# Kernel optimization log

Hardware: AMD Instinct MI355X
Metric: run time of the kernel (lower is better)

The kernel has to match this reference:

```python
import jax, jax.numpy as jnp
import numpy as np

F = 256   # nb_features
H = 8     # nb_heads
B = 4
S = 1024  # q_s == kv_s
SCALE = F ** 0.5  # module MULTIPLIES scores by sqrt(f) when scale=True


def setup_inputs() -> dict:
    key = jax.random.key(0)
    ks = jax.random.split(key, 6)
    return {
        "q_input": jax.random.normal(ks[0], (B, F, S), dtype=jnp.float32),
        "kv_input": jax.random.normal(ks[1], (B, F, S), dtype=jnp.float32),
        "Wq": jax.random.normal(ks[2], (F, F * H), dtype=jnp.float32) * (F ** -0.5),
        "Wk": jax.random.normal(ks[3], (F, F * H), dtype=jnp.float32) * (F ** -0.5),
        "Wv": jax.random.normal(ks[4], (F, F * H), dtype=jnp.float32) * (F ** -0.5),
        "Wz": jax.random.normal(ks[5], (F * H, F), dtype=jnp.float32) * ((F * H) ** -0.5),
    }


def reference(q_input, kv_input, Wq, Wk, Wv, Wz):
    b, f, q_s = q_input.shape
    kv_s = kv_input.shape[2]
    h = H
    # (b, f, s) -> (b, s, f)
    qx = jnp.transpose(q_input, (0, 2, 1))
    kvx = jnp.transpose(kv_input, (0, 2, 1))
    # Linear f -> f*h, then split last dim into (f, h)
    q = (qx @ Wq).reshape(b, q_s, f, h)
    k = (kvx @ Wk).reshape(b, kv_s, f, h)
    v = (kvx @ Wv).reshape(b, kv_s, f, h)
    # sigmoid-gated attention: scores MULTIPLIED by sqrt(f)
    qkt = jnp.einsum('bifh,bjfh->bijh', q, k)
    attn = jax.nn.sigmoid(qkt * SCALE)
    weighted_v = jnp.einsum('bijh,bjfh->bifh', attn, v)  # (b, q_s, f, h)
    z = weighted_v.reshape(b * q_s, f * h)
    out = jax.nn.relu(z @ Wz)  # dropout p=0.0 -> identity
    return jnp.transpose(out.reshape(b, q_s, f), (0, 2, 1))  # (b, f, q_s)
```

## Files before the change

### kernel.cpp

```cpp
#include <hip/hip_runtime.h>
#include <hip/hip_fp16.h>

typedef _Float16 f16;
typedef _Float16 f16x8 __attribute__((ext_vector_type(8)));
typedef float f32x4 __attribute__((ext_vector_type(4)));

#define AS1(p) ((const __attribute__((address_space(1))) void*)(p))
#define AS3(p) ((__attribute__((address_space(3))) void*)(p))

__device__ __forceinline__ void gload16(const void* g, void* l) {
  __builtin_amdgcn_global_load_lds(AS1(g), AS3(l), 16, 0, 0);
}

__global__ __launch_bounds__(256) void tkern(const float* __restrict__ in,
                                             f16* __restrict__ out,
                                             long in_rs, long in_bs,
                                             long out_rs, long out_bs) {
  __shared__ float t[64][68];
  const float* ip = in + blockIdx.z * in_bs + (long)(blockIdx.y * 64) * in_rs + blockIdx.x * 64;
  f16* op = out + blockIdx.z * out_bs + (long)(blockIdx.x * 64) * out_rs + blockIdx.y * 64;
  int tid = threadIdx.x;
  {
    int c4 = (tid & 15) * 4, r0 = tid >> 4;
#pragma unroll
    for (int p = 0; p < 4; ++p) {
      int r = r0 + 16 * p;
      float4 v = *(const float4*)(ip + (long)r * in_rs + c4);
      t[c4 + 0][r] = v.x; t[c4 + 1][r] = v.y; t[c4 + 2][r] = v.z; t[c4 + 3][r] = v.w;
    }
  }
  __syncthreads();
  {
    int r4 = (tid & 15) * 4, c0 = tid >> 4;
#pragma unroll
    for (int p = 0; p < 4; ++p) {
      int c = c0 + 16 * p;
      float4 v = *(const float4*)(&t[c][r4]);
      union { f16 h[4]; unsigned long long u; } pk;
      pk.h[0] = (f16)v.x; pk.h[1] = (f16)v.y; pk.h[2] = (f16)v.z; pk.h[3] = (f16)v.w;
      *(unsigned long long*)(op + (long)c * out_rs + r4) = pk.u;
    }
  }
}

__global__ __launch_bounds__(256) void projk(
    const f16* __restrict__ Xq, const f16* __restrict__ Xkv,
    const f16* __restrict__ Wqt, const f16* __restrict__ Wkt, const f16* __restrict__ Wvt,
    f16* __restrict__ Qh, f16* __restrict__ Kh, f16* __restrict__ Vt) {
  __shared__ char sm[34816];
  int z = blockIdx.z;
  const f16* A = (z == 0) ? Xq : Xkv;
  const f16* B = (z == 0) ? Wqt : (z == 1) ? Wkt : Wvt;
  int m0 = blockIdx.x * 128, n0 = blockIdx.y * 128;
  int tid = threadIdx.x, wave = tid >> 6, lane = tid & 63;
  int wm = wave & 1, wn = wave >> 1;
  char* As = sm;
  char* Bs = sm + 16384;
  f32x4 acc[4][4];
#pragma unroll
  for (int i = 0; i < 4; ++i)
#pragma unroll
    for (int j = 0; j < 4; ++j) acc[i][j] = (f32x4){0.f, 0.f, 0.f, 0.f};

  for (int kt = 0; kt < 4; ++kt) {
    int k0 = kt * 64;
    __syncthreads();
#pragma unroll
    for (int is = 0; is < 4; ++is) {
      int loff = is * 4096 + wave * 1024;
      int g = loff + lane * 16;
      int row = g >> 7, sl = (g >> 4) & 7;
      int sp = (sl ^ (row & 7)) * 8;
      gload16(A + (long)(m0 + row) * 256 + k0 + sp, As + loff);
      gload16(B + (long)(n0 + row) * 256 + k0 + sp, Bs + loff);
    }
    __syncthreads();
#pragma unroll
    for (int t = 0; t < 2; ++t) {
      f16x8 af[4], bf[4];
#pragma unroll
      for (int mi = 0; mi < 4; ++mi) {
        int row = wm * 64 + mi * 16 + (lane & 15);
        int sl = (t * 4 + (lane >> 4)) ^ (row & 7);
        af[mi] = *(const f16x8*)(As + row * 128 + sl * 16);
      }
#pragma unroll
      for (int ni = 0; ni < 4; ++ni) {
        int row = wn * 64 + ni * 16 + (lane & 15);
        int sl = (t * 4 + (lane >> 4)) ^ (row & 7);
        bf[ni] = *(const f16x8*)(Bs + row * 128 + sl * 16);
      }
#pragma unroll
      for (int mi = 0; mi < 4; ++mi)
#pragma unroll
        for (int ni = 0; ni < 4; ++ni)
          acc[mi][ni] = __builtin_amdgcn_mfma_f32_16x16x32_f16(af[mi], bf[ni], acc[mi][ni], 0, 0, 0);
    }
  }
  __syncthreads();
#pragma unroll
  for (int mi = 0; mi < 4; ++mi)
#pragma unroll
    for (int ni = 0; ni < 4; ++ni) {
      int cc = wn * 64 + ni * 16 + (lane & 15);
      int rs0 = wm * 64 + mi * 16 + (lane >> 4) * 4;
      union { f16 h[4]; unsigned long long u; } pk;
#pragma unroll
      for (int r = 0; r < 4; ++r) pk.h[r] = (f16)acc[mi][ni][r];
      *(unsigned long long*)(sm + cc * 272 + rs0 * 2) = pk.u;
    }
  __syncthreads();
  if (z < 2) {
    f16* outp = (z == 0) ? Qh : Kh;
#pragma unroll
    for (int pass = 0; pass < 4; ++pass) {
      int item = pass * 256 + tid;
      int rs = item & 127, h = item >> 7;
      int m = m0 + rs, b = m >> 10, s = m & 1023;
      union { unsigned short u16[16]; uint4 q[2]; } pk;
#pragma unroll
      for (int u = 0; u < 16; ++u)
        pk.u16[u] = *(const unsigned short*)(sm + (h + 8 * u) * 272 + rs * 2);
      f16* dst = outp + ((long)(b * 8 + h) * 1024 + s) * 256 + (n0 >> 3);
      *(uint4*)dst = pk.q[0];
      *(uint4*)(dst + 8) = pk.q[1];
    }
  } else {
    int cc = tid >> 1, half = tid & 1;
    int c = n0 + cc, h = c & 7, fi = c >> 3;
    int m = m0 + half * 64;
    int b = m >> 10, s0 = m & 1023;
    uint4 q[8];
#pragma unroll
    for (int j = 0; j < 8; ++j)
      q[j] = *(const uint4*)(sm + cc * 272 + half * 128 + j * 16);
    f16* dst = Vt + ((long)(b * 8 + h) * 256 + fi) * 1024 + s0;
#pragma unroll
    for (int j = 0; j < 8; ++j) *(uint4*)(dst + j * 8) = q[j];
  }
}

__global__ __launch_bounds__(256) void attnk(
    const f16* __restrict__ Qh, const f16* __restrict__ Kh,
    const f16* __restrict__ Vt, f16* __restrict__ Zb) {
  __shared__ char sm[36864];
  char* Ks = sm;
  char* Vs = sm + 16384;
  char* Ps = sm + 32768;
  int flat = blockIdx.x;
  int xcd = flat & 7, slotb = flat >> 3;
  int bh = xcd + 8 * (slotb & 3);
  int i0 = (slotb >> 2) * 64;
  int tid = threadIdx.x, wave = tid >> 6, lane = tid & 63;
  const f16* Qp = Qh + (long)bh * 262144;
  const f16* Kp = Kh + (long)bh * 262144;
  const f16* Vp = Vt + (long)bh * 262144;
  f16x8 q[8];
  {
    const f16* qr = Qp + (long)(i0 + wave * 16 + (lane & 15)) * 256 + (lane >> 4) * 8;
#pragma unroll
    for (int t = 0; t < 8; ++t) q[t] = *(const f16x8*)(qr + t * 32);
  }
  f32x4 acc[4][4];
#pragma unroll
  for (int i = 0; i < 4; ++i)
#pragma unroll
    for (int j = 0; j < 4; ++j) acc[i][j] = (f32x4){0.f, 0.f, 0.f, 0.f};

  for (int jt = 0; jt < 32; ++jt) {
    int j0 = jt * 32;
    __syncthreads();
#pragma unroll
    for (int is = 0; is < 4; ++is) {
      int loff = is * 4096 + wave * 1024;
      int g = loff + lane * 16;
      {
        int row = g >> 9, sl = (g >> 4) & 31;
        gload16(Kp + (long)(j0 + row) * 256 + ((sl ^ (row & 7)) * 8), Ks + loff);
      }
      {
        int row = g >> 6, sl = (g >> 4) & 3;
        gload16(Vp + (long)row * 1024 + j0 + ((sl ^ ((row >> 1) & 3)) * 8), Vs + loff);
      }
    }
    __syncthreads();
    f32x4 accs[2];
    accs[0] = (f32x4){0.f, 0.f, 0.f, 0.f};
    accs[1] = (f32x4){0.f, 0.f, 0.f, 0.f};
#pragma unroll
    for (int t = 0; t < 8; ++t) {
#pragma unroll
      for (int jf = 0; jf < 2; ++jf) {
        int jr = jf * 16 + (lane & 15);
        int sl = (t * 4 + (lane >> 4)) ^ (jr & 7);
        f16x8 kf = *(const f16x8*)(Ks + jr * 512 + sl * 16);
        accs[jf] = __builtin_amdgcn_mfma_f32_16x16x32_f16(q[t], kf, accs[jf], 0, 0, 0);
      }
    }
#pragma unroll
    for (int jf = 0; jf < 2; ++jf) {
      int j = jf * 16 + (lane & 15);
#pragma unroll
      for (int r = 0; r < 4; ++r) {
        int i = wave * 16 + (lane >> 4) * 4 + r;
        float x = accs[jf][r];
        float p = __builtin_amdgcn_rcpf(1.0f + __builtin_amdgcn_exp2f(x * -23.083120654223414f));
        *(f16*)(Ps + i * 64 + ((j * 2) ^ (((i >> 1) & 3) << 4))) = (f16)p;
      }
    }
    __syncthreads();
    f16x8 pa[4];
#pragma unroll
    for (int mi = 0; mi < 4; ++mi) {
      int ir = mi * 16 + (lane & 15);
      int sl = (lane >> 4) ^ ((ir >> 1) & 3);
      pa[mi] = *(const f16x8*)(Ps + ir * 64 + sl * 16);
    }
#pragma unroll
    for (int nf = 0; nf < 4; ++nf) {
      int fr = wave * 64 + nf * 16 + (lane & 15);
      int sl = (lane >> 4) ^ ((fr >> 1) & 3);
      f16x8 vb = *(const f16x8*)(Vs + fr * 64 + sl * 16);
#pragma unroll
      for (int mi = 0; mi < 4; ++mi)
        acc[mi][nf] = __builtin_amdgcn_mfma_f32_16x16x32_f16(pa[mi], vb, acc[mi][nf], 0, 0, 0);
    }
  }
  f16* zp = Zb + ((long)bh * 1024 + i0) * 256;
#pragma unroll
  for (int mi = 0; mi < 4; ++mi)
#pragma unroll
    for (int nf = 0; nf < 4; ++nf)
#pragma unroll
      for (int r = 0; r < 4; ++r) {
        int i = mi * 16 + (lane >> 4) * 4 + r;
        int f = wave * 64 + nf * 16 + (lane & 15);
        zp[(long)i * 256 + f] = (f16)acc[mi][nf][r];
      }
}

__global__ __launch_bounds__(256) void zkern(
    const f16* __restrict__ Wzt, const f16* __restrict__ Zb,
    float* __restrict__ out) {
  __shared__ char sm[16384];
  char* As = sm;
  char* Bs = sm + 8192;
  int fo0 = blockIdx.x * 64, s0 = blockIdx.y * 64, b = blockIdx.z;
  int tid = threadIdx.x, wave = tid >> 6, lane = tid & 63;
  int wm = wave & 1, wn = wave >> 1;
  f32x4 acc[2][2];
#pragma unroll
  for (int i = 0; i < 2; ++i)
#pragma unroll
    for (int j = 0; j < 2; ++j) acc[i][j] = (f32x4){0.f, 0.f, 0.f, 0.f};

  for (int kt = 0; kt < 32; ++kt) {
    int k0 = kt * 64, h = k0 >> 8, fi0 = k0 & 255;
    __syncthreads();
#pragma unroll
    for (int is = 0; is < 2; ++is) {
      int loff = is * 4096 + wave * 1024;
      int g = loff + lane * 16;
      int row = g >> 7, sl = (g >> 4) & 7;
      int sp = (sl ^ (row & 7)) * 8;
      gload16(Wzt + (long)(fo0 + row) * 2048 + k0 + sp, As + loff);
      gload16(Zb + ((long)(b * 8 + h) * 1024 + s0 + row) * 256 + fi0 + sp, Bs + loff);
    }
    __syncthreads();
#pragma unroll
    for (int t = 0; t < 2; ++t) {
      f16x8 af[2], bf[2];
#pragma unroll
      for (int mi = 0; mi < 2; ++mi) {
        int row = wm * 32 + mi * 16 + (lane & 15);
        int sl = (t * 4 + (lane >> 4)) ^ (row & 7);
        af[mi] = *(const f16x8*)(As + row * 128 + sl * 16);
      }
#pragma unroll
      for (int ni = 0; ni < 2; ++ni) {
        int row = wn * 32 + ni * 16 + (lane & 15);
        int sl = (t * 4 + (lane >> 4)) ^ (row & 7);
        bf[ni] = *(const f16x8*)(Bs + row * 128 + sl * 16);
      }
#pragma unroll
      for (int mi = 0; mi < 2; ++mi)
#pragma unroll
        for (int ni = 0; ni < 2; ++ni)
          acc[mi][ni] = __builtin_amdgcn_mfma_f32_16x16x32_f16(af[mi], bf[ni], acc[mi][ni], 0, 0, 0);
    }
  }
#pragma unroll
  for (int mi = 0; mi < 2; ++mi)
#pragma unroll
    for (int ni = 0; ni < 2; ++ni)
#pragma unroll
      for (int r = 0; r < 4; ++r) {
        int fo = fo0 + wm * 32 + mi * 16 + (lane >> 4) * 4 + r;
        int s = s0 + wn * 32 + ni * 16 + (lane & 15);
        float v = acc[mi][ni][r];
        out[((long)b * 256 + fo) * 1024 + s] = v > 0.f ? v : 0.f;
      }
}

extern "C" void kernel_launch(void* const* d_in, const int* in_sizes, int n_in,
                              void* d_out, int out_size, void* d_ws, size_t ws_size,
                              hipStream_t stream) {
  const float* qin = (const float*)d_in[0];
  const float* kvin = (const float*)d_in[1];
  const float* Wq = (const float*)d_in[2];
  const float* Wk = (const float*)d_in[3];
  const float* Wv = (const float*)d_in[4];
  const float* Wz = (const float*)d_in[5];
  float* out = (float*)d_out;
  char* ws = (char*)d_ws;
  const long MB = 1 << 20;
  f16* Xq  = (f16*)(ws + 0 * MB);
  f16* Xkv = (f16*)(ws + 2 * MB);
  f16* Wqt = (f16*)(ws + 4 * MB);
  f16* Wkt = (f16*)(ws + 5 * MB);
  f16* Wvt = (f16*)(ws + 6 * MB);
  f16* Wzt = (f16*)(ws + 7 * MB);
  f16* Qh  = (f16*)(ws + 8 * MB);
  f16* Kh  = (f16*)(ws + 24 * MB);
  f16* Vt  = (f16*)(ws + 40 * MB);
  f16* Zb  = Qh;
  dim3 blk(256);
  tkern<<<dim3(16, 4, 4), blk, 0, stream>>>(qin, Xq, 1024L, 262144L, 256L, 262144L);
  tkern<<<dim3(16, 4, 4), blk, 0, stream>>>(kvin, Xkv, 1024L, 262144L, 256L, 262144L);
  tkern<<<dim3(32, 4, 1), blk, 0, stream>>>(Wq, Wqt, 2048L, 0L, 256L, 0L);
  tkern<<<dim3(32, 4, 1), blk, 0, stream>>>(Wk, Wkt, 2048L, 0L, 256L, 0L);
  tkern<<<dim3(32, 4, 1), blk, 0, stream>>>(Wv, Wvt, 2048L, 0L, 256L, 0L);
  tkern<<<dim3(4, 4, 8),  blk, 0, stream>>>(Wz, Wzt, 2048L, 256L, 2048L, 256L);
  projk<<<dim3(32, 16, 3), blk, 0, stream>>>(Xq, Xkv, Wqt, Wkt, Wvt, Qh, Kh, Vt);
  attnk<<<dim3(512), blk, 0, stream>>>(Qh, Kh, Vt, Zb);
  zkern<<<dim3(4, 16, 4), blk, 0, stream>>>(Wzt, Zb, out);
}
```

Measured before the change: 138.0 us.

## Double-buffer GEMM/attention tiles, keep P in registers, merge transpose launches

Adds LDS double buffering to the projection, attention and output GEMM kernels, so the next tile's global-to-LDS load overlaps the current tile's MFMAs and each iteration needs one barrier instead of two. The attention kernel is restructured: each wave now owns 16 query rows across all 256 features. The sigmoid probabilities are rearranged into the MFMA A-operand layout with permlane swaps instead of a round trip through LDS, and Z is written out through an LDS-staged coalesced store. The six transpose launches are merged into three. The costs are a larger LDS footprint per block (64KB), which may reduce occupancy, and more accumulator registers in attention.

```diff
diff --git a/kernel.cpp b/kernel.cpp
--- a/kernel.cpp
+++ b/kernel.cpp
@@ -12,13 +12,20 @@
   __builtin_amdgcn_global_load_lds(AS1(g), AS3(l), 16, 0, 0);
 }
 
-__global__ __launch_bounds__(256) void tkern(const float* __restrict__ in,
-                                             f16* __restrict__ out,
-                                             long in_rs, long in_bs,
-                                             long out_rs, long out_bs) {
+__device__ __forceinline__ float sgm(float x) {
+  return __builtin_amdgcn_rcpf(1.0f + __builtin_amdgcn_exp2f(x * -23.083120654223414f));
+}
+
+__device__ __forceinline__ unsigned pack2(float a, float b) {
+  union { f16 h[2]; unsigned u; } x;
+  x.h[0] = (f16)a; x.h[1] = (f16)b;
+  return x.u;
+}
+
+__device__ __forceinline__ void tbody(const float* __restrict__ ip,
+                                      f16* __restrict__ op,
+                                      long in_rs, long out_rs) {
   __shared__ float t[64][68];
-  const float* ip = in + blockIdx.z * in_bs + (long)(blockIdx.y * 64) * in_rs + blockIdx.x * 64;
-  f16* op = out + blockIdx.z * out_bs + (long)(blockIdx.x * 64) * out_rs + blockIdx.y * 64;
   int tid = threadIdx.x;
   {
     int c4 = (tid & 15) * 4, r0 = tid >> 4;
@@ -43,28 +50,60 @@
   }
 }
 
+__global__ __launch_bounds__(256) void tin(const float* __restrict__ qin,
+                                           const float* __restrict__ kvin,
+                                           f16* __restrict__ Xq, f16* __restrict__ Xkv) {
+  int z = blockIdx.z;
+  const float* in = (z < 4) ? qin : kvin;
+  f16* out = (z < 4) ? Xq : Xkv;
+  long b = z & 3;
+  tbody(in + b * 262144 + (long)(blockIdx.y * 64) * 1024 + blockIdx.x * 64,
+        out + b * 262144 + (long)(blockIdx.x * 64) * 256 + blockIdx.y * 64,
+        1024, 256);
+}
+
+__global__ __launch_bounds__(256) void tw3(const float* __restrict__ Wq,
+                                           const float* __restrict__ Wk,
+                                           const float* __restrict__ Wv,
+                                           f16* __restrict__ Wqt, f16* __restrict__ Wkt,
+                                           f16* __restrict__ Wvt) {
+  int z = blockIdx.z;
+  const float* in = (z == 0) ? Wq : (z == 1) ? Wk : Wv;
+  f16* out = (z == 0) ? Wqt : (z == 1) ? Wkt : Wvt;
+  tbody(in + (long)(blockIdx.y * 64) * 2048 + blockIdx.x * 64,
+        out + (long)(blockIdx.x * 64) * 256 + blockIdx.y * 64,
+        2048, 256);
+}
+
+__global__ __launch_bounds__(256) void twz(const float* __restrict__ Wz,
+                                           f16* __restrict__ Wzt) {
+  long z = blockIdx.z;
+  tbody(Wz + z * 256 + (long)(blockIdx.y * 64) * 2048 + blockIdx.x * 64,
+        Wzt + z * 256 + (long)(blockIdx.x * 64) * 2048 + blockIdx.y * 64,
+        2048, 2048);
+}
+
 __global__ __launch_bounds__(256) void projk(
     const f16* __restrict__ Xq, const f16* __restrict__ Xkv,
     const f16* __restrict__ Wqt, const f16* __restrict__ Wkt, const f16* __restrict__ Wvt,
     f16* __restrict__ Qh, f16* __restrict__ Kh, f16* __restrict__ Vt) {
-  __shared__ char sm[34816];
+  __shared__ char sm[65536];
   int z = blockIdx.z;
   const f16* A = (z == 0) ? Xq : Xkv;
   const f16* B = (z == 0) ? Wqt : (z == 1) ? Wkt : Wvt;
   int m0 = blockIdx.x * 128, n0 = blockIdx.y * 128;
   int tid = threadIdx.x, wave = tid >> 6, lane = tid & 63;
   int wm = wave & 1, wn = wave >> 1;
-  char* As = sm;
-  char* Bs = sm + 16384;
   f32x4 acc[4][4];
 #pragma unroll
   for (int i = 0; i < 4; ++i)
 #pragma unroll
     for (int j = 0; j < 4; ++j) acc[i][j] = (f32x4){0.f, 0.f, 0.f, 0.f};
 
-  for (int kt = 0; kt < 4; ++kt) {
+  auto PSTAGE = [&](int buf, int kt) {
+    char* As = sm + buf * 32768;
+    char* Bs = As + 16384;
     int k0 = kt * 64;
-    __syncthreads();
 #pragma unroll
     for (int is = 0; is < 4; ++is) {
       int loff = is * 4096 + wave * 1024;
@@ -74,7 +113,15 @@
       gload16(A + (long)(m0 + row) * 256 + k0 + sp, As + loff);
       gload16(B + (long)(n0 + row) * 256 + k0 + sp, Bs + loff);
     }
-    __syncthreads();
+  };
+
+  PSTAGE(0, 0);
+  __syncthreads();
+  for (int kt = 0; kt < 4; ++kt) {
+    int cur = kt & 1;
+    if (kt < 3) PSTAGE(cur ^ 1, kt + 1);
+    const char* As = sm + cur * 32768;
+    const char* Bs = As + 16384;
 #pragma unroll
     for (int t = 0; t < 2; ++t) {
       f16x8 af[4], bf[4];
@@ -96,8 +143,8 @@
         for (int ni = 0; ni < 4; ++ni)
           acc[mi][ni] = __builtin_amdgcn_mfma_f32_16x16x32_f16(af[mi], bf[ni], acc[mi][ni], 0, 0, 0);
     }
-  }
-  __syncthreads();
+    __syncthreads();
+  }
 #pragma unroll
   for (int mi = 0; mi < 4; ++mi)
 #pragma unroll
@@ -143,33 +190,29 @@
 __global__ __launch_bounds__(256) void attnk(
     const f16* __restrict__ Qh, const f16* __restrict__ Kh,
     const f16* __restrict__ Vt, f16* __restrict__ Zb) {
-  __shared__ char sm[36864];
-  char* Ks = sm;
-  char* Vs = sm + 16384;
-  char* Ps = sm + 32768;
+  __shared__ char sm[65536];
   int flat = blockIdx.x;
   int xcd = flat & 7, slotb = flat >> 3;
   int bh = xcd + 8 * (slotb & 3);
   int i0 = (slotb >> 2) * 64;
   int tid = threadIdx.x, wave = tid >> 6, lane = tid & 63;
+  int l15 = lane & 15, l4 = lane >> 4;
   const f16* Qp = Qh + (long)bh * 262144;
   const f16* Kp = Kh + (long)bh * 262144;
   const f16* Vp = Vt + (long)bh * 262144;
   f16x8 q[8];
   {
-    const f16* qr = Qp + (long)(i0 + wave * 16 + (lane & 15)) * 256 + (lane >> 4) * 8;
+    const f16* qr = Qp + (long)(i0 + wave * 16 + l15) * 256 + l4 * 8;
 #pragma unroll
     for (int t = 0; t < 8; ++t) q[t] = *(const f16x8*)(qr + t * 32);
   }
-  f32x4 acc[4][4];
-#pragma unroll
-  for (int i = 0; i < 4; ++i)
-#pragma unroll
-    for (int j = 0; j < 4; ++j) acc[i][j] = (f32x4){0.f, 0.f, 0.f, 0.f};
-
-  for (int jt = 0; jt < 32; ++jt) {
-    int j0 = jt * 32;
-    __syncthreads();
+  f32x4 acc[16];
+#pragma unroll
+  for (int i = 0; i < 16; ++i) acc[i] = (f32x4){0.f, 0.f, 0.f, 0.f};
+
+  auto STAGE = [&](int buf, int j0) {
+    char* Ks = sm + buf * 32768;
+    char* Vs = Ks + 16384;
 #pragma unroll
     for (int is = 0; is < 4; ++is) {
       int loff = is * 4096 + wave * 1024;
@@ -183,68 +226,67 @@
         gload16(Vp + (long)row * 1024 + j0 + ((sl ^ ((row >> 1) & 3)) * 8), Vs + loff);
       }
     }
+  };
+
+  STAGE(0, 0);
+  __syncthreads();
+  for (int jt = 0; jt < 32; ++jt) {
+    int cur = jt & 1;
+    if (jt < 31) STAGE(cur ^ 1, (jt + 1) * 32);
+    const char* Ks = sm + cur * 32768;
+    const char* Vs = Ks + 16384;
+    f32x4 s0 = (f32x4){0.f, 0.f, 0.f, 0.f};
+    f32x4 s1 = (f32x4){0.f, 0.f, 0.f, 0.f};
+#pragma unroll
+    for (int t = 0; t < 8; ++t) {
+      int sl = (t * 4 + l4) ^ (l15 & 7);
+      f16x8 k0 = *(const f16x8*)(Ks + l15 * 512 + sl * 16);
+      f16x8 k1 = *(const f16x8*)(Ks + (16 + l15) * 512 + sl * 16);
+      s0 = __builtin_amdgcn_mfma_f32_16x16x32_f16(k0, q[t], s0, 0, 0, 0);
+      s1 = __builtin_amdgcn_mfma_f32_16x16x32_f16(k1, q[t], s1, 0, 0, 0);
+    }
+    unsigned u00 = pack2(sgm(s0[0]), sgm(s0[1]));
+    unsigned u01 = pack2(sgm(s0[2]), sgm(s0[3]));
+    unsigned u10 = pack2(sgm(s1[0]), sgm(s1[1]));
+    unsigned u11 = pack2(sgm(s1[2]), sgm(s1[3]));
+    auto a0 = __builtin_amdgcn_permlane32_swap(u00, u10, false, false);
+    auto w02 = __builtin_amdgcn_permlane16_swap(a0[0], a0[1], false, false);
+    auto a1 = __builtin_amdgcn_permlane32_swap(u01, u11, false, false);
+    auto w13 = __builtin_amdgcn_permlane16_swap(a1[0], a1[1], false, false);
+    union { unsigned u[4]; f16x8 v; } pa;
+    pa.u[0] = w02[0]; pa.u[1] = w13[0]; pa.u[2] = w02[1]; pa.u[3] = w13[1];
+#pragma unroll
+    for (int nf = 0; nf < 16; ++nf) {
+      int fr = nf * 16 + l15;
+      int sl = l4 ^ ((fr >> 1) & 3);
+      f16x8 vb = *(const f16x8*)(Vs + fr * 64 + sl * 16);
+      acc[nf] = __builtin_amdgcn_mfma_f32_16x16x32_f16(pa.v, vb, acc[nf], 0, 0, 0);
+    }
     __syncthreads();
-    f32x4 accs[2];
-    accs[0] = (f32x4){0.f, 0.f, 0.f, 0.f};
-    accs[1] = (f32x4){0.f, 0.f, 0.f, 0.f};
-#pragma unroll
-    for (int t = 0; t < 8; ++t) {
-#pragma unroll
-      for (int jf = 0; jf < 2; ++jf) {
-        int jr = jf * 16 + (lane & 15);
-        int sl = (t * 4 + (lane >> 4)) ^ (jr & 7);
-        f16x8 kf = *(const f16x8*)(Ks + jr * 512 + sl * 16);
-        accs[jf] = __builtin_amdgcn_mfma_f32_16x16x32_f16(q[t], kf, accs[jf], 0, 0, 0);
-      }
-    }
-#pragma unroll
-    for (int jf = 0; jf < 2; ++jf) {
-      int j = jf * 16 + (lane & 15);
-#pragma unroll
-      for (int r = 0; r < 4; ++r) {
-        int i = wave * 16 + (lane >> 4) * 4 + r;
-        float x = accs[jf][r];
-        float p = __builtin_amdgcn_rcpf(1.0f + __builtin_amdgcn_exp2f(x * -23.083120654223414f));
-        *(f16*)(Ps + i * 64 + ((j * 2) ^ (((i >> 1) & 3) << 4))) = (f16)p;
-      }
-    }
-    __syncthreads();
-    f16x8 pa[4];
-#pragma unroll
-    for (int mi = 0; mi < 4; ++mi) {
-      int ir = mi * 16 + (lane & 15);
-      int sl = (lane >> 4) ^ ((ir >> 1) & 3);
-      pa[mi] = *(const f16x8*)(Ps + ir * 64 + sl * 16);
-    }
-#pragma unroll
-    for (int nf = 0; nf < 4; ++nf) {
-      int fr = wave * 64 + nf * 16 + (lane & 15);
-      int sl = (lane >> 4) ^ ((fr >> 1) & 3);
-      f16x8 vb = *(const f16x8*)(Vs + fr * 64 + sl * 16);
-#pragma unroll
-      for (int mi = 0; mi < 4; ++mi)
-        acc[mi][nf] = __builtin_amdgcn_mfma_f32_16x16x32_f16(pa[mi], vb, acc[mi][nf], 0, 0, 0);
-    }
-  }
+  }
+#pragma unroll
+  for (int nf = 0; nf < 16; ++nf)
+#pragma unroll
+    for (int r = 0; r < 4; ++r) {
+      int il = wave * 16 + l4 * 4 + r;
+      int f = nf * 16 + l15;
+      *(f16*)(sm + il * 512 + ((f * 2) ^ (((il >> 2) & 3) << 5))) = (f16)acc[nf][r];
+    }
+  __syncthreads();
   f16* zp = Zb + ((long)bh * 1024 + i0) * 256;
 #pragma unroll
-  for (int mi = 0; mi < 4; ++mi)
-#pragma unroll
-    for (int nf = 0; nf < 4; ++nf)
-#pragma unroll
-      for (int r = 0; r < 4; ++r) {
-        int i = mi * 16 + (lane >> 4) * 4 + r;
-        int f = wave * 64 + nf * 16 + (lane & 15);
-        zp[(long)i * 256 + f] = (f16)acc[mi][nf][r];
-      }
+  for (int c = 0; c < 8; ++c) {
+    int il = c * 8 + (tid >> 5);
+    int fb = (tid & 31) * 16;
+    uint4 v = *(const uint4*)(sm + il * 512 + (fb ^ (((il >> 2) & 3) << 5)));
+    *(uint4*)((char*)zp + il * 512 + fb) = v;
+  }
 }
 
 __global__ __launch_bounds__(256) void zkern(
     const f16* __restrict__ Wzt, const f16* __restrict__ Zb,
     float* __restrict__ out) {
-  __shared__ char sm[16384];
-  char* As = sm;
-  char* Bs = sm + 8192;
+  __shared__ char sm[32768];
   int fo0 = blockIdx.x * 64, s0 = blockIdx.y * 64, b = blockIdx.z;
   int tid = threadIdx.x, wave = tid >> 6, lane = tid & 63;
   int wm = wave & 1, wn = wave >> 1;
@@ -254,9 +296,10 @@
 #pragma unroll
     for (int j = 0; j < 2; ++j) acc[i][j] = (f32x4){0.f, 0.f, 0.f, 0.f};
 
-  for (int kt = 0; kt < 32; ++kt) {
+  auto ZSTAGE = [&](int buf, int kt) {
+    char* As = sm + buf * 16384;
+    char* Bs = As + 8192;
     int k0 = kt * 64, h = k0 >> 8, fi0 = k0 & 255;
-    __syncthreads();
 #pragma unroll
     for (int is = 0; is < 2; ++is) {
       int loff = is * 4096 + wave * 1024;
@@ -266,7 +309,15 @@
       gload16(Wzt + (long)(fo0 + row) * 2048 + k0 + sp, As + loff);
       gload16(Zb + ((long)(b * 8 + h) * 1024 + s0 + row) * 256 + fi0 + sp, Bs + loff);
     }
-    __syncthreads();
+  };
+
+  ZSTAGE(0, 0);
+  __syncthreads();
+  for (int kt = 0; kt < 32; ++kt) {
+    int cur = kt & 1;
+    if (kt < 31) ZSTAGE(cur ^ 1, kt + 1);
+    const char* As = sm + cur * 16384;
+    const char* Bs = As + 8192;
 #pragma unroll
     for (int t = 0; t < 2; ++t) {
       f16x8 af[2], bf[2];
@@ -288,6 +339,7 @@
         for (int ni = 0; ni < 2; ++ni)
           acc[mi][ni] = __builtin_amdgcn_mfma_f32_16x16x32_f16(af[mi], bf[ni], acc[mi][ni], 0, 0, 0);
     }
+    __syncthreads();
   }
 #pragma unroll
   for (int mi = 0; mi < 2; ++mi)
@@ -325,12 +377,9 @@
   f16* Vt  = (f16*)(ws + 40 * MB);
   f16* Zb  = Qh;
   dim3 blk(256);
-  tkern<<<dim3(16, 4, 4), blk, 0, stream>>>(qin, Xq, 1024L, 262144L, 256L, 262144L);
-  tkern<<<dim3(16, 4, 4), blk, 0, stream>>>(kvin, Xkv, 1024L, 262144L, 256L, 262144L);
-  tkern<<<dim3(32, 4, 1), blk, 0, stream>>>(Wq, Wqt, 2048L, 0L, 256L, 0L);
-  tkern<<<dim3(32, 4, 1), blk, 0, stream>>>(Wk, Wkt, 2048L, 0L, 256L, 0L);
-  tkern<<<dim3(32, 4, 1), blk, 0, stream>>>(Wv, Wvt, 2048L, 0L, 256L, 0L);
-  tkern<<<dim3(4, 4, 8),  blk, 0, stream>>>(Wz, Wzt, 2048L, 256L, 2048L, 256L);
+  tin<<<dim3(16, 4, 8), blk, 0, stream>>>(qin, kvin, Xq, Xkv);
+  tw3<<<dim3(32, 4, 3), blk, 0, stream>>>(Wq, Wk, Wv, Wqt, Wkt, Wvt);
+  twz<<<dim3(4, 4, 8), blk, 0, stream>>>(Wz, Wzt);
   projk<<<dim3(32, 16, 3), blk, 0, stream>>>(Xq, Xkv, Wqt, Wkt, Wvt, Qh, Kh, Vt);
   attnk<<<dim3(512), blk, 0, stream>>>(Qh, Kh, Vt, Zb);
   zkern<<<dim3(4, 16, 4), blk, 0, stream>>>(Wzt, Zb, out);
```

After: 126.3 us. -8.4%, faster.
